# Optimization experiments

Hardware: AMD Instinct MI355X
Metric: run time of the kernel (lower is better)

The kernel has to match this reference:

```python
import jax, jax.numpy as jnp
import numpy as np
import math

N_QUBITS = 10
N_VQC_LAYERS = 3
N_ACTIONS = 3
B = 4096
T = 128
D = 1 << N_QUBITS
IU, JU = np.triu_indices(N_QUBITS, 1)  # combinations(range(N),2) order


def _ry(a):
    # [B] (or scalar) -> [...,2,2] complex64 RY(a)
    c, s = jnp.cos(a * 0.5), jnp.sin(a * 0.5)
    return jnp.stack([jnp.stack([c, -s], -1), jnp.stack([s, c], -1)], -2).astype(jnp.complex64)


def _rz(a):
    h = a.astype(jnp.complex64) * 0.5
    z = jnp.zeros_like(h)
    return jnp.stack([jnp.stack([jnp.exp(-1j * h), z], -1), jnp.stack([z, jnp.exp(1j * h)], -1)], -2)


def _rot(w):
    # Rot(phi,theta,omega) = RZ(omega) @ RY(theta) @ RZ(phi); w=[phi,theta,omega]
    return _rz(w[2]) @ _ry(w[1]) @ _rz(w[0])


def _apply_1q(state, gate, q, n):
    # apply 2x2 gate to qubit q of [B, 2^n] state (bit q has stride 2^(n-q-1))
    b, d = state.shape
    lo = 1 << (n - q - 1)
    hi = 1 << q
    s = state.reshape(b, hi, 2, lo)
    if gate.ndim == 3:
        s = jnp.einsum('bij,bhjl->bhil', gate, s)
    else:
        s = jnp.einsum('ij,bhjl->bhil', gate, s)
    return s.reshape(b, d)


def _static_tables(n, n_layers):
    s = np.arange(1 << n)
    # IsingZZ sign masks: +1 if bits differ, -1 if equal (matches torch buffer)
    masks = np.stack([
        np.where(((s >> (n - 1 - qi)) & 1) ^ ((s >> (n - 1 - qj)) & 1) == 1, 1.0, -1.0)
        for qi, qj in zip(IU, JU)
    ]).astype(np.float32)
    # PauliZ expectation signs per qubit
    zsigns = np.where(((s[None, :] >> (n - 1 - np.arange(n)[:, None])) & 1) == 0, 1.0, -1.0).astype(np.float32)
    # CNOT ring as index permutations (same math as the dense matmul in torch)
    perms = []
    for l in range(n_layers):
        rng = l % (n - 1) + 1 if n > 1 else 1
        layer = []
        for ctrl in range(n):
            tgt = (ctrl + rng) % n
            cb = (s >> (n - 1 - ctrl)) & 1
            layer.append(np.where(cb == 1, s ^ (1 << (n - 1 - tgt)), s))
        perms.append(layer)
    return masks, zsigns, perms


MASKS, ZSIGNS, PERMS = _static_tables(N_QUBITS, N_VQC_LAYERS)


def setup_inputs() -> dict:
    key = jax.random.key(0)
    k1, k2, k3, k4 = jax.random.split(key, 4)
    return {
        'c_kt': jax.random.normal(k1, (B, T, N_QUBITS), jnp.float32),
        'delta_c_kt': jax.random.normal(k2, (B, T, N_QUBITS), jnp.float32),
        'vqc_weights': jax.random.normal(k3, (N_VQC_LAYERS, N_QUBITS, 3), jnp.float32),
        'w_proj': jax.random.normal(k4, (N_ACTIONS, N_QUBITS), jnp.float32) / math.sqrt(N_QUBITS),
        'b_proj': jnp.zeros((N_ACTIONS,), jnp.float32),
        'log_alpha': jnp.zeros((), jnp.float32),
    }


def reference(c_kt, delta_c_kt, vqc_weights, w_proj, b_proj, log_alpha):
    n, L = N_QUBITS, N_VQC_LAYERS
    b, t, k_ = c_kt.shape
    # --- IsingCouplingEstimator: Pearson corr -> tanh(rho * alpha), zero diag ---
    feat = c_kt + 0.5 * delta_c_kt
    X = jnp.swapaxes(feat, 1, 2)                      # [B, K, T]
    Xc = X - X.mean(-1, keepdims=True)
    std = jnp.maximum(jnp.sqrt((Xc * Xc).sum(-1, keepdims=True) / (t - 1)), 1e-8)
    Xn = Xc / std
    rho = jnp.einsum('bit,bjt->bij', Xn, Xn) / (t - 1)
    rho = rho * (1.0 - jnp.eye(k_, dtype=rho.dtype))
    J = jnp.tanh(rho * jnp.exp(log_alpha))            # [B, K, K]
    j_upper = J[:, IU, JU]                            # [B, K*(K-1)/2]

    # --- angle encoding from last timestep ---
    theta = c_kt[:, -1, :]                            # [B, K]
    phi = delta_c_kt[:, -1, :]

    # --- TorchVQC state-vector simulation ---
    state = jnp.zeros((b, D), jnp.complex64).at[:, 0].set(1.0 + 0j)
    for q in range(n):
        state = _apply_1q(state, _ry(theta[:, q]), q, n)
        state = _apply_1q(state, _rz(phi[:, q]), q, n)
    # all IsingZZ phases fused: exp(0.5j * pi * sum_p J_p * mask_p)
    ang = math.pi * (j_upper @ jnp.asarray(MASKS))    # [B, D]
    state = state * jnp.exp(0.5j * ang.astype(jnp.complex64))
    for l in range(L):
        for q in range(n):
            state = _apply_1q(state, _rot(vqc_weights[l, q]), q, n)
        for q in range(n):
            state = state[:, PERMS[l][q]]             # CNOT as permutation
        if l < L - 1:                                 # data re-uploading
            for q in range(n):
                state = _apply_1q(state, _ry(theta[:, q] * 0.5), q, n)
                state = _apply_1q(state, _rz(phi[:, q] * 0.5), q, n)
    probs = jnp.real(state) ** 2 + jnp.imag(state) ** 2
    expvals = probs @ jnp.asarray(ZSIGNS).T           # [B, N] <Z_k>

    # --- logit projection ---
    return expvals @ w_proj.T + b_proj                # [B, n_actions]
```

## Files before the change

kernel.cpp:

```cpp
#include <hip/hip_runtime.h>


typedef float v2 __attribute__((ext_vector_type(2)));

template<int CTRL>
__device__ __forceinline__ float dppf(float v) {
  return __int_as_float(__builtin_amdgcn_update_dpp(
      0, __float_as_int(v), CTRL, 0xF, 0xF, true));
}

template<int LM>
__device__ __forceinline__ float xshfl(float v) {
  if constexpr (LM == 1) {
    return dppf<0xB1>(v);
  } else if constexpr (LM == 2) {
    return dppf<0x4E>(v);
  } else if constexpr (LM == 4) {
    return dppf<0x141>(dppf<0x1B>(v));
  } else if constexpr (LM == 8) {
    return dppf<0x128>(v);
  } else if constexpr (LM == 16) {
    return __int_as_float(__builtin_amdgcn_ds_swizzle(__float_as_int(v), 0x401F));
  } else {
    return __shfl_xor(v, 32);
  }
}

template<int LM>
__device__ __forceinline__ v2 xshfl2(v2 v) {
  v2 r; r.x = xshfl<LM>(v.x); r.y = xshfl<LM>(v.y); return r;
}

template<int B, int NP>
__device__ __forceinline__ void fstage(float* p, int lane) {
  #pragma unroll
  for (int i = 0; i < NP; ++i) {
    const float send = (lane & B) ? p[i] : p[i + NP];
    const float recv = xshfl<B>(send);
    const float keep = (lane & B) ? p[i + NP] : p[i];
    p[i] = keep + recv;
  }
}

constexpr int holder_lane45(int v) {
  const int a = v >= 24; int r = v - 24 * a;
  const int b = r >= 12; r -= 12 * b;
  const int c = r >= 6;  r -= 6 * c;
  const int d = r >= 3;  r -= 3 * d;
  const int e = r >= 2;  r -= 2 * e;
  return a | (b << 1) | (c << 2) | (d << 3) | (e << 4) | (r << 5);
}

constexpr int holder_lane10(int v) {
  const int a = v >= 5; int r = v - 5 * a;
  const int b = r >= 3; r -= 3 * b;
  const int c = r >= 2; r -= 2 * c;
  return a | (b << 1) | (c << 2) | (r << 3);
}

__device__ __forceinline__ void funnel10(float* p, int lane) {
  fstage<1, 5>(p, lane);
  p[5] = 0.0f;
  fstage<2, 3>(p, lane);
  p[3] = 0.0f;
  fstage<4, 2>(p, lane);
  fstage<8, 1>(p, lane);
  p[0] += xshfl<16>(p[0]);
  p[0] += xshfl<32>(p[0]);
}

__device__ __forceinline__ float rfl(float x) {
  return __int_as_float(__builtin_amdgcn_readfirstlane(__float_as_int(x)));
}

#define RLg(g_, x_) __int_as_float(__builtin_amdgcn_readlane(__float_as_int(x_), (g_)))

__device__ __forceinline__ float fast_tanh(float x) {
  return 1.0f - 2.0f / (__expf(2.0f * x) + 1.0f);
}

__device__ __forceinline__ v2 sneg(v2 a) {
  v2 r; r.x = -a.y; r.y = a.x; return r;
}

template<int BIT>
__device__ __forceinline__ void gate_apply(v2 (&st)[16], int lane,
    float m00r, float m00i, float m01r, float m01i,
    float m10r, float m10i, float m11r, float m11i) {
  if constexpr (BIT < 4) {
    #pragma unroll
    for (int r0 = 0; r0 < 16; ++r0) {
      if ((r0 & (1 << BIT)) == 0) {
        const int r1 = r0 | (1 << BIT);
        const v2 a0 = st[r0], a1 = st[r1];
        const v2 s0 = sneg(a0), s1 = sneg(a1);
        st[r0] = m00r*a0 + m00i*s0 + m01r*a1 + m01i*s1;
        st[r1] = m10r*a0 + m10i*s0 + m11r*a1 + m11i*s1;
      }
    }
  } else {
    constexpr int lm = 1 << (BIT - 4);
    const bool hi = (lane & lm) != 0;
    const float cAr = hi ? m11r : m00r, cAi = hi ? m11i : m00i;
    const float cBr = hi ? m10r : m01r, cBi = hi ? m10i : m01i;
    #pragma unroll
    for (int r = 0; r < 16; ++r) {
      const v2 p = xshfl2<lm>(st[r]);
      const v2 a = st[r];
      st[r] = cAr*a + cAi*sneg(a) + cBr*p + cBi*sneg(p);
    }
  }
}

template<int CB, int TB>
__device__ __forceinline__ void cnot_apply(v2 (&st)[16], int lane) {
  if constexpr (CB >= 4 && TB >= 4) {
    constexpr int lm = 1 << (TB - 4);
    const bool c1 = (lane & (1 << (CB - 4))) != 0;
    #pragma unroll
    for (int r = 0; r < 16; ++r) {
      const v2 p = xshfl2<lm>(st[r]);
      st[r].x = c1 ? p.x : st[r].x;
      st[r].y = c1 ? p.y : st[r].y;
    }
  } else if constexpr (CB >= 4 && TB < 4) {
    const bool c1 = (lane & (1 << (CB - 4))) != 0;
    #pragma unroll
    for (int r0 = 0; r0 < 16; ++r0) {
      if ((r0 & (1 << TB)) == 0) {
        const int r1 = r0 | (1 << TB);
        const v2 a = st[r0], b = st[r1];
        st[r0].x = c1 ? b.x : a.x;  st[r0].y = c1 ? b.y : a.y;
        st[r1].x = c1 ? a.x : b.x;  st[r1].y = c1 ? a.y : b.y;
      }
    }
  } else if constexpr (CB < 4 && TB >= 4) {
    constexpr int lm = 1 << (TB - 4);
    #pragma unroll
    for (int r = 0; r < 16; ++r) {
      if ((r & (1 << CB)) != 0) {
        st[r] = xshfl2<lm>(st[r]);
      }
    }
  } else {
    #pragma unroll
    for (int r0 = 0; r0 < 16; ++r0) {
      if ((r0 & (1 << CB)) != 0 && (r0 & (1 << TB)) == 0) {
        const int r1 = r0 | (1 << TB);
        const v2 t = st[r0]; st[r0] = st[r1]; st[r1] = t;
      }
    }
  }
}

template<int I, int J>
__device__ __forceinline__ void pair_accum(float t, int lane, float& Cc,
                                           float (&dcf)[4], float (&ecf)[6]) {
  if constexpr (J <= 5) {
    const bool diff = (((lane >> (5 - I)) ^ (lane >> (5 - J))) & 1) != 0;
    Cc += diff ? -t : t;
  } else if constexpr (I <= 5) {
    const bool b = ((lane >> (5 - I)) & 1) != 0;
    dcf[J - 6] += b ? -t : t;
  } else {
    constexpr int eb = (I == 6) ? 0 : (I == 7) ? 3 : 5;
    ecf[eb + (J - I - 1)] = t;
  }
}

#define PACC(v_, i_, j_) pair_accum<i_, j_>(RLg(holder_lane45(v_), tl), lane, Cc, dcoef, ecoef);

#define GATE(g_, q_) \
  gate_apply<9 - (q_)>(st, lane, \
      RLg(g_, Mr00), RLg(g_, Mi00), RLg(g_, Mr01), RLg(g_, Mi01), \
      RLg(g_, Mr10), RLg(g_, Mi10), RLg(g_, Mr11), RLg(g_, Mi11));

#define CNOT(ctrl, rng) cnot_apply<9 - (ctrl), 9 - ((((ctrl) + (rng)) % 10))>(st, lane);

extern "C" __global__ void __launch_bounds__(256, 2)
qhl_kernel(const float* __restrict__ c_kt, const float* __restrict__ dc_kt,
           const float* __restrict__ vw,  const float* __restrict__ w_proj,
           const float* __restrict__ b_proj, const float* __restrict__ log_alpha,
           float* __restrict__ out) {
  const int wave = threadIdx.x >> 6;
  const int lane = threadIdx.x & 63;
  const int bid  = blockIdx.x * 4 + wave;

  const float* c   = c_kt  + (size_t)bid * 1280;
  const float* dcp = dc_kt + (size_t)bid * 1280;

  float Mr00, Mi00, Mr01, Mi01, Mr10, Mi10, Mr11, Mi11;
  {
    const int g = lane < 30 ? lane : 0;
    const int l = g / 10, q = g - l * 10;
    const float w0 = vw[g*3+0], w1 = vw[g*3+1], w2 = vw[g*3+2];
    float cY, sY; __sincosf(0.5f*w1, &sY, &cY);
    float ca, sa; __sincosf(0.5f*(w0+w2), &sa, &ca);
    float cb, sb; __sincosf(0.5f*(w0-w2), &sb, &cb);
    const float r00r =  cY*ca, r00i = -cY*sa, r01r = -sY*cb, r01i = -sY*sb;
    const float r10r =  sY*cb, r10i = -sY*sb, r11r =  cY*ca, r11i =  cY*sa;
    if (l == 0) {
      Mr00 = r00r; Mi00 = r00i; Mr01 = r01r; Mi01 = r01i;
      Mr10 = r10r; Mi10 = r10i; Mr11 = r11r; Mi11 = r11i;
    } else {
      const float thq = c[1270 + q], phq = dcp[1270 + q];
      float cy, sy; __sincosf(0.25f * thq, &sy, &cy);
      float cz, sz; __sincosf(0.25f * phq, &sz, &cz);
      const float e00r =  cy*cz, e00i = -cy*sz, e01r = -sy*cz, e01i =  sy*sz;
      const float e10r =  sy*cz, e10i =  sy*sz, e11r =  cy*cz, e11i =  cy*sz;
      Mr00 = r00r*e00r - r00i*e00i + r01r*e10r - r01i*e10i;
      Mi00 = r00r*e00i + r00i*e00r + r01r*e10i + r01i*e10r;
      Mr01 = r00r*e01r - r00i*e01i + r01r*e11r - r01i*e11i;
      Mi01 = r00r*e01i + r00i*e01r + r01r*e11i + r01i*e11r;
      Mr10 = r10r*e00r - r10i*e00i + r11r*e10r - r11i*e10i;
      Mi10 = r10r*e00i + r10i*e00r + r11r*e10i + r11i*e10r;
      Mr11 = r10r*e01r - r10i*e01i + r11r*e11r - r11i*e11i;
      Mi11 = r10r*e01i + r10i*e01r + r11r*e11i + r11i*e11r;
    }
  }

  v2 ym[10];
  {
    const float2* c0 = (const float2*)(c   + lane * 10);
    const float2* d0 = (const float2*)(dcp + lane * 10);
    const float2* c1 = (const float2*)(c   + (lane + 64) * 10);
    const float2* d1 = (const float2*)(dcp + (lane + 64) * 10);
    #pragma unroll
    for (int k = 0; k < 5; ++k) {
      const float2 a0 = c0[k], b0 = d0[k], a1 = c1[k], b1 = d1[k];
      ym[2*k].x   = a0.x + 0.5f * b0.x;  ym[2*k].y   = a1.x + 0.5f * b1.x;
      ym[2*k+1].x = a0.y + 0.5f * b0.y;  ym[2*k+1].y = a1.y + 0.5f * b1.y;
    }
  }

  {
    float mb[6];
    float m10[10];
    #pragma unroll
    for (int k = 0; k < 10; ++k) m10[k] = ym[k].x + ym[k].y;
    #pragma unroll
    for (int i = 0; i < 5; ++i) {
      const float send = (lane & 1) ? m10[i] : m10[i + 5];
      const float recv = xshfl<1>(send);
      const float keep = (lane & 1) ? m10[i + 5] : m10[i];
      mb[i] = keep + recv;
    }
    mb[5] = 0.0f;
    fstage<2, 3>(mb, lane);
    mb[3] = 0.0f;
    fstage<4, 2>(mb, lane);
    fstage<8, 1>(mb, lane);
    mb[0] += xshfl<16>(mb[0]);
    mb[0] += xshfl<32>(mb[0]);
    mb[0] *= (1.0f / 128.0f);
    #pragma unroll
    for (int k = 0; k < 10; ++k) {
      const float mk = RLg(holder_lane10(k), mb[0]);
      ym[k].x -= mk; ym[k].y -= mk;
    }
    float s10[10];
    #pragma unroll
    for (int k = 0; k < 10; ++k) { const v2 sq = ym[k] * ym[k]; s10[k] = sq.x + sq.y; }
    #pragma unroll
    for (int i = 0; i < 5; ++i) {
      const float send = (lane & 1) ? s10[i] : s10[i + 5];
      const float recv = xshfl<1>(send);
      const float keep = (lane & 1) ? s10[i + 5] : s10[i];
      mb[i] = keep + recv;
    }
    mb[5] = 0.0f;
    fstage<2, 3>(mb, lane);
    mb[3] = 0.0f;
    fstage<4, 2>(mb, lane);
    fstage<8, 1>(mb, lane);
    mb[0] += xshfl<16>(mb[0]);
    mb[0] += xshfl<32>(mb[0]);
    const float rsv = fminf(__builtin_amdgcn_rsqf(mb[0] * (1.0f / 127.0f)), 1e8f);
    #pragma unroll
    for (int k = 0; k < 10; ++k) {
      const float rk = RLg(holder_lane10(k), rsv);
      ym[k].x *= rk; ym[k].y *= rk;
    }
  }

  const float expA = rfl(__expf(log_alpha[0]));
  float Cc = 0.0f, dcoef[4] = {0, 0, 0, 0}, ecoef[6];
  float tl;
  {
    constexpr int PI_[45] = {0,0,0,0,0,0,0,0,0, 1,1,1,1,1,1,1,1, 2,2,2,2,2,2,2,
                             3,3,3,3,3,3, 4,4,4,4,4, 5,5,5,5, 6,6,6, 7,7, 8};
    constexpr int PJ_[45] = {1,2,3,4,5,6,7,8,9, 2,3,4,5,6,7,8,9, 3,4,5,6,7,8,9,
                             4,5,6,7,8,9, 5,6,7,8,9, 6,7,8,9, 7,8,9, 8,9, 9};
    float p[48];
    #pragma unroll
    for (int v = 0; v < 45; ++v) {
      const v2 pr = ym[PI_[v]] * ym[PJ_[v]];
      p[v] = pr.x + pr.y;
    }
    p[45] = 0.0f; p[46] = 0.0f; p[47] = 0.0f;
    fstage<1, 24>(p, lane);
    fstage<2, 12>(p, lane);
    fstage<4, 6>(p, lane);
    fstage<8, 3>(p, lane);
    p[3] = 0.0f;
    fstage<16, 2>(p, lane);
    fstage<32, 1>(p, lane);
    const float sc = expA * (1.0f / 127.0f);
    tl = -1.5707963267948966f * fast_tanh(p[0] * sc);
  }
  PACC(0,0,1) PACC(1,0,2) PACC(2,0,3) PACC(3,0,4) PACC(4,0,5) PACC(5,0,6) PACC(6,0,7) PACC(7,0,8) PACC(8,0,9)
  PACC(9,1,2) PACC(10,1,3) PACC(11,1,4) PACC(12,1,5) PACC(13,1,6) PACC(14,1,7) PACC(15,1,8) PACC(16,1,9)
  PACC(17,2,3) PACC(18,2,4) PACC(19,2,5) PACC(20,2,6) PACC(21,2,7) PACC(22,2,8) PACC(23,2,9)
  PACC(24,3,4) PACC(25,3,5) PACC(26,3,6) PACC(27,3,7) PACC(28,3,8) PACC(29,3,9)
  PACC(30,4,5) PACC(31,4,6) PACC(32,4,7) PACC(33,4,8) PACC(34,4,9)
  PACC(35,5,6) PACC(36,5,7) PACC(37,5,8) PACC(38,5,9)
  PACC(39,6,7) PACC(40,6,8) PACC(41,6,9)
  PACC(42,7,8) PACC(43,7,9)
  PACC(44,8,9)

  float th[10], ph[10];
  #pragma unroll
  for (int q = 0; q < 10; ++q) {
    th[q] = rfl(c[1270 + q]);
    ph[q] = rfl(dcp[1270 + q]);
  }

  float Rr_l, Ri_l;
  {
    const int rr = lane & 15;
    float prr = 1.0f, pri = 0.0f;
    #pragma unroll
    for (int t = 0; t < 4; ++t) {
      float cy, sy; __sincosf(0.5f * th[6 + t], &sy, &cy);
      float cz, sz; __sincosf(0.5f * ph[6 + t], &sz, &cz);
      const bool b = ((rr >> (3 - t)) & 1) != 0;
      const float fr = b ? sy * cz : cy * cz;
      const float fi = b ? sy * sz : -cy * sz;
      const float nr = prr * fr - pri * fi;
      pri = prr * fi + pri * fr;
      prr = nr;
    }
    Rr_l = prr; Ri_l = pri;
  }

  v2 st[16];
  {
    v2 L; L.x = 1.0f; L.y = 0.0f;
    #pragma unroll
    for (int q = 0; q < 6; ++q) {
      float cy, sy; __sincosf(0.5f * th[q], &sy, &cy);
      float cz, sz; __sincosf(0.5f * ph[q], &sz, &cz);
      const bool b = ((lane >> (5 - q)) & 1) != 0;
      const float zr = b ? sy * cz : cy * cz;
      const float zi = b ? sy * sz : -cy * sz;
      L = zr * L + zi * sneg(L);
    }
    #pragma unroll
    for (int r = 0; r < 16; ++r) {
      const int b3 = (r >> 3) & 1, b2 = (r >> 2) & 1, b1 = (r >> 1) & 1, b0 = r & 1;
      const float Rr = RLg(r, Rr_l);
      const float Ri = RLg(r, Ri_l);
      float h = Cc;
      h += b3 ? -dcoef[0] : dcoef[0];
      h += b2 ? -dcoef[1] : dcoef[1];
      h += b1 ? -dcoef[2] : dcoef[2];
      h += b0 ? -dcoef[3] : dcoef[3];
      h += (b3 ^ b2) ? -ecoef[0] : ecoef[0];
      h += (b3 ^ b1) ? -ecoef[1] : ecoef[1];
      h += (b3 ^ b0) ? -ecoef[2] : ecoef[2];
      h += (b2 ^ b1) ? -ecoef[3] : ecoef[3];
      h += (b2 ^ b0) ? -ecoef[4] : ecoef[4];
      h += (b1 ^ b0) ? -ecoef[5] : ecoef[5];
      float sn, cs; __sincosf(h, &sn, &cs);
      const v2 p = cs * L + sn * sneg(L);
      st[r] = Rr * p + Ri * sneg(p);
    }
  }

  GATE(0,0) GATE(1,1) GATE(2,2) GATE(3,3) GATE(4,4)
  GATE(5,5) GATE(6,6) GATE(7,7) GATE(8,8) GATE(9,9)
  CNOT(0,1) CNOT(1,1) CNOT(2,1) CNOT(3,1) CNOT(4,1)
  CNOT(5,1) CNOT(6,1) CNOT(7,1) CNOT(8,1) CNOT(9,1)
  GATE(10,0) GATE(11,1) GATE(12,2) GATE(13,3) GATE(14,4)
  GATE(15,5) GATE(16,6) GATE(17,7) GATE(18,8) GATE(19,9)
  CNOT(0,2) CNOT(1,2) CNOT(2,2) CNOT(3,2) CNOT(4,2)
  CNOT(5,2) CNOT(6,2) CNOT(7,2) CNOT(8,2) CNOT(9,2)
  GATE(20,0) GATE(21,1) GATE(22,2) GATE(23,3) GATE(24,4)
  GATE(25,5) GATE(26,6) GATE(27,7) GATE(28,8) GATE(29,9)
  CNOT(0,3) CNOT(1,3) CNOT(2,3) CNOT(3,3) CNOT(4,3)
  CNOT(5,3) CNOT(6,3) CNOT(7,3) CNOT(8,3) CNOT(9,3)

  float P = 0.0f, e6 = 0.0f, e7 = 0.0f, e8 = 0.0f, e9 = 0.0f;
  #pragma unroll
  for (int r = 0; r < 16; ++r) {
    const v2 sq = st[r] * st[r];
    const float pp = sq.x + sq.y;
    P  += pp;
    e6 += (r & 8) ? -pp : pp;
    e7 += (r & 4) ? -pp : pp;
    e8 += (r & 2) ? -pp : pp;
    e9 += (r & 1) ? -pp : pp;
  }
  float mv[10];
  mv[0] = (lane & 32) ? -P : P;
  mv[1] = (lane & 16) ? -P : P;
  mv[2] = (lane &  8) ? -P : P;
  mv[3] = (lane &  4) ? -P : P;
  mv[4] = (lane &  2) ? -P : P;
  mv[5] = (lane &  1) ? -P : P;
  mv[6] = e6; mv[7] = e7; mv[8] = e8; mv[9] = e9;
  {
    float fb[6];
    #pragma unroll
    for (int i = 0; i < 5; ++i) {
      const float send = (lane & 1) ? mv[i] : mv[i + 5];
      const float recv = xshfl<1>(send);
      const float keep = (lane & 1) ? mv[i + 5] : mv[i];
      fb[i] = keep + recv;
    }
    fb[5] = 0.0f;
    fstage<2, 3>(fb, lane);
    fb[3] = 0.0f;
    fstage<4, 2>(fb, lane);
    fstage<8, 1>(fb, lane);
    fb[0] += xshfl<16>(fb[0]);
    fb[0] += xshfl<32>(fb[0]);
    float ev[10];
    #pragma unroll
    for (int k = 0; k < 10; ++k) ev[k] = RLg(holder_lane10(k), fb[0]);
    if (lane < 3) {
      float acc = b_proj[lane];
      #pragma unroll
      for (int i = 0; i < 10; ++i) acc += w_proj[lane * 10 + i] * ev[i];
      out[(size_t)bid * 3 + lane] = acc;
    }
  }
}

extern "C" void kernel_launch(void* const* d_in, const int* in_sizes, int n_in,
                              void* d_out, int out_size, void* d_ws, size_t ws_size,
                              hipStream_t stream) {
  (void)in_sizes; (void)n_in; (void)d_ws; (void)ws_size; (void)out_size;
  const float* c_kt      = (const float*)d_in[0];
  const float* dc_kt     = (const float*)d_in[1];
  const float* vw        = (const float*)d_in[2];
  const float* w_proj    = (const float*)d_in[3];
  const float* b_proj    = (const float*)d_in[4];
  const float* log_alpha = (const float*)d_in[5];
  float* out = (float*)d_out;
  qhl_kernel<<<dim3(1024), dim3(256), 0, stream>>>(c_kt, dc_kt, vw, w_proj,
                                                   b_proj, log_alpha, out);
}
```

Baseline: 131.0 us.

## Eliminate CNOT ring layers by tracking the accumulated linear basis permutation

Removes all 30 explicit CNOT permutation stages. Each CNOT block is a GF(2)-linear map on basis indices, so the kernel composes these maps at compile time and conjugates the following single-qubit gates through them. Each gate then becomes a pairing of amplitudes along an arbitrary XOR mask, with parity-dependent coefficient signs. The final Z-expectation signs are taken from the accumulated map instead of plain bits. This saves the shuffle and select work of the CNOTs, but gates may now need multi-bit cross-lane exchanges (chained DPP, swizzle or bpermute), which cost more per gate.

```diff
diff --git a/kernel.cpp b/kernel.cpp
--- a/kernel.cpp
+++ b/kernel.cpp
@@ -2,6 +2,35 @@
 
 
 typedef float v2 __attribute__((ext_vector_type(2)));
+
+struct M10 { unsigned row[10]; };
+constexpr M10 mident() { M10 m{}; for (int i=0;i<10;++i) m.row[i]=1u<<i; return m; }
+constexpr M10 mmul(M10 A, M10 B) {
+  M10 C{};
+  for (int i=0;i<10;++i){ unsigned x=0; for (int j=0;j<10;++j) if ((A.row[i]>>j)&1u) x ^= B.row[j]; C.row[i]=x; }
+  return C;
+}
+constexpr M10 cnotT(int ctrl, int rng) {
+  const int tgt = (ctrl + rng) % 10;
+  const int cb = 9 - ctrl, tb = 9 - tgt;
+  M10 m = mident(); m.row[tb] = (1u<<tb)|(1u<<cb); return m;
+}
+constexpr M10 blockPinv(int rng) { M10 m = cnotT(0,rng); for (int c=1;c<10;++c) m = mmul(m, cnotT(c,rng)); return m; }
+constexpr M10 blockP(int rng)    { M10 m = cnotT(9,rng); for (int c=8;c>=0;--c) m = mmul(m, cnotT(c,rng)); return m; }
+constexpr unsigned mcol(M10 A, int c) { unsigned x=0; for (int i=0;i<10;++i) x |= ((A.row[i]>>c)&1u)<<i; return x; }
+constexpr int par(unsigned x){ int p=0; for (int i=0;i<10;++i) p ^= (int)((x>>i)&1u); return p; }
+constexpr int topbit4(int x){ int b=0; for (int i=1;i<4;++i) if (x>>i) b=i; return 1<<b; }
+
+constexpr M10 Q1  = blockP(1);
+constexpr M10 Q1i = blockPinv(1);
+constexpr M10 Q2  = mmul(blockP(2), Q1);
+constexpr M10 Q2i = mmul(Q1i, blockPinv(2));
+constexpr M10 Q3  = mmul(blockP(3), Q2);
+
+static_assert(mmul(Q1, Q1i).row[0]==1u && mmul(Q1,Q1i).row[9]==(1u<<9), "inv1");
+static_assert(mmul(Q2, Q2i).row[0]==1u && mmul(Q2,Q2i).row[7]==(1u<<7), "inv2");
+static_assert(par(mcol(Q1i,0)&Q1.row[0]) && par(mcol(Q1i,5)&Q1.row[5]) && par(mcol(Q1i,9)&Q1.row[9]), "dual1");
+static_assert(par(mcol(Q2i,0)&Q2.row[0]) && par(mcol(Q2i,4)&Q2.row[4]) && par(mcol(Q2i,9)&Q2.row[9]), "dual2");
 
 template<int CTRL>
 __device__ __forceinline__ float dppf(float v) {
@@ -9,26 +38,30 @@
       0, __float_as_int(v), CTRL, 0xF, 0xF, true));
 }
 
+template<int MASK>
+__device__ __forceinline__ float xany(float v, int baddr) {
+  constexpr int QC[4] = {0, 0xB1, 0x4E, 0x1B};
+  if constexpr (MASK == 0) return v;
+  else if constexpr (MASK <= 3) return dppf<QC[MASK]>(v);
+  else if constexpr (MASK == 4) return dppf<0x141>(dppf<0x1B>(v));
+  else if constexpr (MASK == 8) return dppf<0x128>(v);
+  else if constexpr (MASK >= 9 && MASK <= 11) return dppf<QC[MASK&3]>(dppf<0x128>(v));
+  else if constexpr (MASK < 32) return __int_as_float(__builtin_amdgcn_ds_swizzle(__float_as_int(v), (MASK<<10)|0x1F));
+  else return __int_as_float(__builtin_amdgcn_ds_bpermute(baddr, __float_as_int(v)));
+}
+template<int MASK>
+__device__ __forceinline__ v2 xany2(v2 v, int baddr) {
+  v2 r; r.x = xany<MASK>(v.x, baddr); r.y = xany<MASK>(v.y, baddr); return r;
+}
+
 template<int LM>
 __device__ __forceinline__ float xshfl(float v) {
-  if constexpr (LM == 1) {
-    return dppf<0xB1>(v);
-  } else if constexpr (LM == 2) {
-    return dppf<0x4E>(v);
-  } else if constexpr (LM == 4) {
-    return dppf<0x141>(dppf<0x1B>(v));
-  } else if constexpr (LM == 8) {
-    return dppf<0x128>(v);
-  } else if constexpr (LM == 16) {
-    return __int_as_float(__builtin_amdgcn_ds_swizzle(__float_as_int(v), 0x401F));
-  } else {
-    return __shfl_xor(v, 32);
-  }
-}
-
-template<int LM>
-__device__ __forceinline__ v2 xshfl2(v2 v) {
-  v2 r; r.x = xshfl<LM>(v.x); r.y = xshfl<LM>(v.y); return r;
+  if constexpr (LM == 1) return dppf<0xB1>(v);
+  else if constexpr (LM == 2) return dppf<0x4E>(v);
+  else if constexpr (LM == 4) return dppf<0x141>(dppf<0x1B>(v));
+  else if constexpr (LM == 8) return dppf<0x128>(v);
+  else if constexpr (LM == 16) return __int_as_float(__builtin_amdgcn_ds_swizzle(__float_as_int(v), 0x401F));
+  else return __shfl_xor(v, 32);
 }
 
 template<int B, int NP>
@@ -41,7 +74,6 @@
     p[i] = keep + recv;
   }
 }
-
 constexpr int holder_lane45(int v) {
   const int a = v >= 24; int r = v - 24 * a;
   const int b = r >= 12; r -= 12 * b;
@@ -50,7 +82,6 @@
   const int e = r >= 2;  r -= 2 * e;
   return a | (b << 1) | (c << 2) | (d << 3) | (e << 4) | (r << 5);
 }
-
 constexpr int holder_lane10(int v) {
   const int a = v >= 5; int r = v - 5 * a;
   const int b = r >= 3; r -= 3 * b;
@@ -58,96 +89,57 @@
   return a | (b << 1) | (c << 2) | (r << 3);
 }
 
-__device__ __forceinline__ void funnel10(float* p, int lane) {
-  fstage<1, 5>(p, lane);
-  p[5] = 0.0f;
-  fstage<2, 3>(p, lane);
-  p[3] = 0.0f;
-  fstage<4, 2>(p, lane);
-  fstage<8, 1>(p, lane);
-  p[0] += xshfl<16>(p[0]);
-  p[0] += xshfl<32>(p[0]);
-}
-
 __device__ __forceinline__ float rfl(float x) {
   return __int_as_float(__builtin_amdgcn_readfirstlane(__float_as_int(x)));
 }
-
 #define RLg(g_, x_) __int_as_float(__builtin_amdgcn_readlane(__float_as_int(x_), (g_)))
 
 __device__ __forceinline__ float fast_tanh(float x) {
   return 1.0f - 2.0f / (__expf(2.0f * x) + 1.0f);
 }
-
 __device__ __forceinline__ v2 sneg(v2 a) {
   v2 r; r.x = -a.y; r.y = a.x; return r;
 }
 
-template<int BIT>
-__device__ __forceinline__ void gate_apply(v2 (&st)[16], int lane,
-    float m00r, float m00i, float m01r, float m01i,
-    float m10r, float m10i, float m11r, float m11i) {
-  if constexpr (BIT < 4) {
-    #pragma unroll
-    for (int r0 = 0; r0 < 16; ++r0) {
-      if ((r0 & (1 << BIT)) == 0) {
-        const int r1 = r0 | (1 << BIT);
-        const v2 a0 = st[r0], a1 = st[r1];
-        const v2 s0 = sneg(a0), s1 = sneg(a1);
-        st[r0] = m00r*a0 + m00i*s0 + m01r*a1 + m01i*s1;
-        st[r1] = m10r*a0 + m10i*s0 + m11r*a1 + m11i*s1;
-      }
+template<int M, int V>
+__device__ __forceinline__ void gate_g(v2 (&st)[16], int lane,
+                                       float ar, float ai, float br, float bi) {
+  constexpr int MR = M & 15, ML = (M >> 4) & 63;
+  constexpr int VR = V & 15, VL = (V >> 4) & 63;
+  bool hl = false;
+  if constexpr (VL != 0) hl = (__builtin_popcount(lane & VL) & 1) != 0;
+  const float aiX = hl ? -ai : ai;
+  const float brX = hl ? -br : br;
+  int baddr = 0;
+  if constexpr (ML >= 32) baddr = (lane ^ ML) << 2;
+  if constexpr (MR == 0) {
+    #pragma unroll
+    for (int r = 0; r < 16; ++r) {
+      const v2 p = xany2<ML>(st[r], baddr);
+      const v2 a = st[r];
+      if ((__builtin_popcount(r & VR) & 1) == 0)
+        st[r] = ar*a + aiX*sneg(a) + brX*p + bi*sneg(p);
+      else
+        st[r] = ar*a - aiX*sneg(a) - brX*p + bi*sneg(p);
     }
   } else {
-    constexpr int lm = 1 << (BIT - 4);
-    const bool hi = (lane & lm) != 0;
-    const float cAr = hi ? m11r : m00r, cAi = hi ? m11i : m00i;
-    const float cBr = hi ? m10r : m01r, cBi = hi ? m10i : m01i;
+    constexpr int HB = topbit4(MR);
     #pragma unroll
     for (int r = 0; r < 16; ++r) {
-      const v2 p = xshfl2<lm>(st[r]);
-      const v2 a = st[r];
-      st[r] = cAr*a + cAi*sneg(a) + cBr*p + cBi*sneg(p);
-    }
-  }
-}
-
-template<int CB, int TB>
-__device__ __forceinline__ void cnot_apply(v2 (&st)[16], int lane) {
-  if constexpr (CB >= 4 && TB >= 4) {
-    constexpr int lm = 1 << (TB - 4);
-    const bool c1 = (lane & (1 << (CB - 4))) != 0;
-    #pragma unroll
-    for (int r = 0; r < 16; ++r) {
-      const v2 p = xshfl2<lm>(st[r]);
-      st[r].x = c1 ? p.x : st[r].x;
-      st[r].y = c1 ? p.y : st[r].y;
-    }
-  } else if constexpr (CB >= 4 && TB < 4) {
-    const bool c1 = (lane & (1 << (CB - 4))) != 0;
-    #pragma unroll
-    for (int r0 = 0; r0 < 16; ++r0) {
-      if ((r0 & (1 << TB)) == 0) {
-        const int r1 = r0 | (1 << TB);
-        const v2 a = st[r0], b = st[r1];
-        st[r0].x = c1 ? b.x : a.x;  st[r0].y = c1 ? b.y : a.y;
-        st[r1].x = c1 ? a.x : b.x;  st[r1].y = c1 ? a.y : b.y;
-      }
-    }
-  } else if constexpr (CB < 4 && TB >= 4) {
-    constexpr int lm = 1 << (TB - 4);
-    #pragma unroll
-    for (int r = 0; r < 16; ++r) {
-      if ((r & (1 << CB)) != 0) {
-        st[r] = xshfl2<lm>(st[r]);
-      }
-    }
-  } else {
-    #pragma unroll
-    for (int r0 = 0; r0 < 16; ++r0) {
-      if ((r0 & (1 << CB)) != 0 && (r0 & (1 << TB)) == 0) {
-        const int r1 = r0 | (1 << TB);
-        const v2 t = st[r0]; st[r0] = st[r1]; st[r1] = t;
+      if ((r & HB) == 0) {
+        const int r1 = r ^ MR;
+        v2 pa, pb;
+        if constexpr (ML == 0) { pa = st[r1]; pb = st[r]; }
+        else { pa = xany2<ML>(st[r1], baddr); pb = xany2<ML>(st[r], baddr); }
+        const v2 a = st[r], b = st[r1];
+        if ((__builtin_popcount(r & VR) & 1) == 0)
+          st[r] = ar*a + aiX*sneg(a) + brX*pa + bi*sneg(pa);
+        else
+          st[r] = ar*a - aiX*sneg(a) - brX*pa + bi*sneg(pa);
+        if ((__builtin_popcount(r1 & VR) & 1) == 0)
+          st[r1] = ar*b + aiX*sneg(b) + brX*pb + bi*sneg(pb);
+        else
+          st[r1] = ar*b - aiX*sneg(b) - brX*pb + bi*sneg(pb);
       }
     }
   }
@@ -167,15 +159,14 @@
     ecf[eb + (J - I - 1)] = t;
   }
 }
-
 #define PACC(v_, i_, j_) pair_accum<i_, j_>(RLg(holder_lane45(v_), tl), lane, Cc, dcoef, ecoef);
 
-#define GATE(g_, q_) \
-  gate_apply<9 - (q_)>(st, lane, \
-      RLg(g_, Mr00), RLg(g_, Mi00), RLg(g_, Mr01), RLg(g_, Mi01), \
-      RLg(g_, Mr10), RLg(g_, Mi10), RLg(g_, Mr11), RLg(g_, Mi11));
-
-#define CNOT(ctrl, rng) cnot_apply<9 - (ctrl), 9 - ((((ctrl) + (rng)) % 10))>(st, lane);
+#define GATE0(g_, q_) gate_g<(1<<(9-(q_))), (1<<(9-(q_)))>(st, lane, \
+    RLg(g_,Mr00), RLg(g_,Mi00), RLg(g_,Mr01), RLg(g_,Mi01));
+#define GATE1(g_, q_) gate_g<(int)mcol(Q1i,9-(q_)), (int)Q1.row[9-(q_)]>(st, lane, \
+    RLg(g_,Mr00), RLg(g_,Mi00), RLg(g_,Mr01), RLg(g_,Mi01));
+#define GATE2(g_, q_) gate_g<(int)mcol(Q2i,9-(q_)), (int)Q2.row[9-(q_)]>(st, lane, \
+    RLg(g_,Mr00), RLg(g_,Mi00), RLg(g_,Mr01), RLg(g_,Mi01));
 
 extern "C" __global__ void __launch_bounds__(256, 2)
 qhl_kernel(const float* __restrict__ c_kt, const float* __restrict__ dc_kt,
@@ -189,7 +180,7 @@
   const float* c   = c_kt  + (size_t)bid * 1280;
   const float* dcp = dc_kt + (size_t)bid * 1280;
 
-  float Mr00, Mi00, Mr01, Mi01, Mr10, Mi10, Mr11, Mi11;
+  float Mr00, Mi00, Mr01, Mi01;
   {
     const int g = lane < 30 ? lane : 0;
     const int l = g / 10, q = g - l * 10;
@@ -198,10 +189,8 @@
     float ca, sa; __sincosf(0.5f*(w0+w2), &sa, &ca);
     float cb, sb; __sincosf(0.5f*(w0-w2), &sb, &cb);
     const float r00r =  cY*ca, r00i = -cY*sa, r01r = -sY*cb, r01i = -sY*sb;
-    const float r10r =  sY*cb, r10i = -sY*sb, r11r =  cY*ca, r11i =  cY*sa;
     if (l == 0) {
       Mr00 = r00r; Mi00 = r00i; Mr01 = r01r; Mi01 = r01i;
-      Mr10 = r10r; Mi10 = r10i; Mr11 = r11r; Mi11 = r11i;
     } else {
       const float thq = c[1270 + q], phq = dcp[1270 + q];
       float cy, sy; __sincosf(0.25f * thq, &sy, &cy);
@@ -212,10 +201,6 @@
       Mi00 = r00r*e00i + r00i*e00r + r01r*e10i + r01i*e10r;
       Mr01 = r00r*e01r - r00i*e01i + r01r*e11r - r01i*e11i;
       Mi01 = r00r*e01i + r00i*e01r + r01r*e11i + r01i*e11r;
-      Mr10 = r10r*e00r - r10i*e00i + r11r*e10r - r11i*e10i;
-      Mi10 = r10r*e00i + r10i*e00r + r11r*e10i + r11i*e10r;
-      Mr11 = r10r*e01r - r10i*e01i + r11r*e11r - r11i*e11i;
-      Mi11 = r10r*e01i + r10i*e01r + r11r*e11i + r11i*e11r;
     }
   }
 
@@ -235,14 +220,14 @@
 
   {
     float mb[6];
-    float m10[10];
-    #pragma unroll
-    for (int k = 0; k < 10; ++k) m10[k] = ym[k].x + ym[k].y;
+    float m10a[10];
+    #pragma unroll
+    for (int k = 0; k < 10; ++k) m10a[k] = ym[k].x + ym[k].y;
     #pragma unroll
     for (int i = 0; i < 5; ++i) {
-      const float send = (lane & 1) ? m10[i] : m10[i + 5];
+      const float send = (lane & 1) ? m10a[i] : m10a[i + 5];
       const float recv = xshfl<1>(send);
-      const float keep = (lane & 1) ? m10[i + 5] : m10[i];
+      const float keep = (lane & 1) ? m10a[i + 5] : m10a[i];
       mb[i] = keep + recv;
     }
     mb[5] = 0.0f;
@@ -377,38 +362,31 @@
     }
   }
 
-  GATE(0,0) GATE(1,1) GATE(2,2) GATE(3,3) GATE(4,4)
-  GATE(5,5) GATE(6,6) GATE(7,7) GATE(8,8) GATE(9,9)
-  CNOT(0,1) CNOT(1,1) CNOT(2,1) CNOT(3,1) CNOT(4,1)
-  CNOT(5,1) CNOT(6,1) CNOT(7,1) CNOT(8,1) CNOT(9,1)
-  GATE(10,0) GATE(11,1) GATE(12,2) GATE(13,3) GATE(14,4)
-  GATE(15,5) GATE(16,6) GATE(17,7) GATE(18,8) GATE(19,9)
-  CNOT(0,2) CNOT(1,2) CNOT(2,2) CNOT(3,2) CNOT(4,2)
-  CNOT(5,2) CNOT(6,2) CNOT(7,2) CNOT(8,2) CNOT(9,2)
-  GATE(20,0) GATE(21,1) GATE(22,2) GATE(23,3) GATE(24,4)
-  GATE(25,5) GATE(26,6) GATE(27,7) GATE(28,8) GATE(29,9)
-  CNOT(0,3) CNOT(1,3) CNOT(2,3) CNOT(3,3) CNOT(4,3)
-  CNOT(5,3) CNOT(6,3) CNOT(7,3) CNOT(8,3) CNOT(9,3)
-
-  float P = 0.0f, e6 = 0.0f, e7 = 0.0f, e8 = 0.0f, e9 = 0.0f;
+  GATE0(0,0) GATE0(1,1) GATE0(2,2) GATE0(3,3) GATE0(4,4)
+  GATE0(5,5) GATE0(6,6) GATE0(7,7) GATE0(8,8) GATE0(9,9)
+  GATE1(10,0) GATE1(11,1) GATE1(12,2) GATE1(13,3) GATE1(14,4)
+  GATE1(15,5) GATE1(16,6) GATE1(17,7) GATE1(18,8) GATE1(19,9)
+  GATE2(20,0) GATE2(21,1) GATE2(22,2) GATE2(23,3) GATE2(24,4)
+  GATE2(25,5) GATE2(26,6) GATE2(27,7) GATE2(28,8) GATE2(29,9)
+
+  float e[10] = {0,0,0,0,0,0,0,0,0,0};
   #pragma unroll
   for (int r = 0; r < 16; ++r) {
     const v2 sq = st[r] * st[r];
     const float pp = sq.x + sq.y;
-    P  += pp;
-    e6 += (r & 8) ? -pp : pp;
-    e7 += (r & 4) ? -pp : pp;
-    e8 += (r & 2) ? -pp : pp;
-    e9 += (r & 1) ? -pp : pp;
+    #pragma unroll
+    for (int q = 0; q < 10; ++q) {
+      const bool s = (__builtin_popcount(r & (int)(Q3.row[9-q] & 15u)) & 1) != 0;
+      e[q] += s ? -pp : pp;
+    }
   }
   float mv[10];
-  mv[0] = (lane & 32) ? -P : P;
-  mv[1] = (lane & 16) ? -P : P;
-  mv[2] = (lane &  8) ? -P : P;
-  mv[3] = (lane &  4) ? -P : P;
-  mv[4] = (lane &  2) ? -P : P;
-  mv[5] = (lane &  1) ? -P : P;
-  mv[6] = e6; mv[7] = e7; mv[8] = e8; mv[9] = e9;
+  #pragma unroll
+  for (int q = 0; q < 10; ++q) {
+    const int wl = (int)((Q3.row[9-q] >> 4) & 63u);
+    const bool sl = wl ? ((__builtin_popcount(lane & wl) & 1) != 0) : false;
+    mv[q] = sl ? -e[q] : e[q];
+  }
   {
     float fb[6];
     #pragma unroll
```

Result: faster. 126.6 us (-3.4%).
